# Optimization experiments

Measured on AMD Instinct MI355X. Metric: run time of the kernel, lower is better.

## Reference

```python
import jax, jax.numpy as jnp
import numpy as np

T, Z, Y, X = 16, 16, 16, 16
NS, NC = 4, 3
D = NS * NC  # 12 internal (spin*color) components
DIAG = 4.5   # 4 + mass
OUT_PARITY = 0


def _r_masks():
    t = jnp.arange(T).reshape(T, 1, 1, 1, 1)
    z = jnp.arange(Z).reshape(1, Z, 1, 1, 1)
    y = jnp.arange(Y).reshape(1, 1, Y, 1, 1)
    r = (t + z + y + OUT_PARITY) % 2
    r = jnp.broadcast_to(r, (T, Z, Y, X // 2, D))
    return r == 1, r == 0  # fwd mask, bwd mask


def _cmatvec(Kr, Ki, vr, vi):
    # complex (K) @ (v) per site; K: [T,Z,Y,X/2,D,D], v: [T,Z,Y,X/2,D]
    ar = jnp.einsum('tzyxij,tzyxj->tzyxi', Kr, vr) - jnp.einsum('tzyxij,tzyxj->tzyxi', Ki, vi)
    ai = jnp.einsum('tzyxij,tzyxj->tzyxi', Kr, vi) + jnp.einsum('tzyxij,tzyxj->tzyxi', Ki, vr)
    return ar, ai


def setup_inputs() -> dict:
    key = jax.random.key(0)
    ks = jax.random.split(key, 6)
    shp_psi = (T, Z, Y, X // 2, NS, NC)
    shp_K = (4, T, Z, Y, X // 2, D, D)
    return {
        'psi_re': jax.random.normal(ks[0], shp_psi, dtype=jnp.float32),
        'psi_im': jax.random.normal(ks[1], shp_psi, dtype=jnp.float32),
        'K_fwd_re': jax.random.normal(ks[2], shp_K, dtype=jnp.float32),
        'K_fwd_im': jax.random.normal(ks[3], shp_K, dtype=jnp.float32),
        'K_bwd_re': jax.random.normal(ks[4], shp_K, dtype=jnp.float32),
        'K_bwd_im': jax.random.normal(ks[5], shp_K, dtype=jnp.float32),
    }


def reference(psi_re, psi_im, K_fwd_re, K_fwd_im, K_bwd_re, K_bwd_im):
    pr = psi_re.reshape(T, Z, Y, X // 2, D)
    pi = psi_im.reshape(T, Z, Y, X // 2, D)
    mask_f, mask_b = _r_masks()
    out_re = DIAG * pr
    out_im = DIAG * pi
    for mu in range(4):
        ax = mu  # ldim = mu - 5 on a rank-5 tensor == axis mu
        if mu < 3:
            pf_re = jnp.roll(pr, -1, axis=ax); pf_im = jnp.roll(pi, -1, axis=ax)
            pb_re = jnp.roll(pr, 1, axis=ax); pb_im = jnp.roll(pi, 1, axis=ax)
        else:
            # staggered X hop on the half-lattice, selected by parity masks
            pf_re = jnp.where(mask_f, jnp.roll(pr, -1, axis=ax), pr)
            pf_im = jnp.where(mask_f, jnp.roll(pi, -1, axis=ax), pi)
            pb_re = jnp.where(mask_b, jnp.roll(pr, 1, axis=ax), pr)
            pb_im = jnp.where(mask_b, jnp.roll(pi, 1, axis=ax), pi)
        cf_re, cf_im = _cmatvec(K_fwd_re[mu], K_fwd_im[mu], pf_re, pf_im)
        cb_re, cb_im = _cmatvec(K_bwd_re[mu], K_bwd_im[mu], pb_re, pb_im)
        out_re = out_re - 0.5 * (cf_re + cb_re)
        out_im = out_im - 0.5 * (cf_im + cb_im)
    return (out_re.reshape(T, Z, Y, X // 2, NS, NC),
            out_im.reshape(T, Z, Y, X // 2, NS, NC))
```

## Files before the change

### kernel.cpp

```cpp
#include <hip/hip_runtime.h>

#define TD 16
#define ZD 16
#define YD 16
#define XH 8
#define DD 12
#define NSITES (TD*ZD*YD*XH)
#define SPB 16
#define THREADS (SPB*DD)
#define DIAG 4.5f
#define VSTRIDE 100

__global__ __launch_bounds__(THREADS) void hop_kernel(
    const float* __restrict__ psi_re, const float* __restrict__ psi_im,
    const float* __restrict__ K_fwd_re, const float* __restrict__ K_fwd_im,
    const float* __restrict__ K_bwd_re, const float* __restrict__ K_bwd_im,
    float* __restrict__ out_re, float* __restrict__ out_im)
{
    __shared__ float vre[SPB][VSTRIDE];
    __shared__ float vim[SPB][VSTRIDE];
    __shared__ int   nidx[SPB][8];

    const int tid   = threadIdx.x;
    const int site0 = blockIdx.x * SPB;

    if (tid < SPB * 8) {
        const int s = tid >> 3, c = tid & 7;
        const int sg = site0 + s;
        const int x = sg & 7, y = (sg >> 3) & 15, z = (sg >> 7) & 15, t = (sg >> 11) & 15;
        const int r = (t + z + y) & 1;
        int nt = t, nz = z, ny = y, nx = x;
        switch (c) {
            case 0: nt = (t + 1)  & 15; break;
            case 1: nt = (t + 15) & 15; break;
            case 2: nz = (z + 1)  & 15; break;
            case 3: nz = (z + 15) & 15; break;
            case 4: ny = (y + 1)  & 15; break;
            case 5: ny = (y + 15) & 15; break;
            case 6: if (r == 1) nx = (x + 1) & 7; break;
            case 7: if (r == 0) nx = (x + 7) & 7; break;
        }
        nidx[s][c] = ((nt * 16 + nz) * 16 + ny) * 8 + nx;
    }
    __syncthreads();

    for (int e = tid; e < SPB * 8 * DD; e += THREADS) {
        const int j  = e % 12;
        const int sc = e / 12;
        const int s  = sc >> 3, c = sc & 7;
        const int n  = nidx[s][c];
        vre[s][c * 12 + j] = psi_re[n * 12 + j];
        vim[s][c * 12 + j] = psi_im[n * 12 + j];
    }
    __syncthreads();

    const int s    = tid / 12;
    const int i    = tid - s * 12;
    const int site = site0 + s;

    const float pr_c = psi_re[site * 12 + i];
    const float pi_c = psi_im[site * 12 + i];
    float o_re = DIAG * pr_c;
    float o_im = DIAG * pi_c;

    #pragma unroll 2
    for (int c = 0; c < 8; ++c) {
        const int mu = c >> 1;
        const float* __restrict__ Kr_arr = (c & 1) ? K_bwd_re : K_fwd_re;
        const float* __restrict__ Ki_arr = (c & 1) ? K_bwd_im : K_fwd_im;
        const int off = (mu * NSITES + site) * 144 + i * 12;
        const float4* Kr4 = (const float4*)(Kr_arr + off);
        const float4* Ki4 = (const float4*)(Ki_arr + off);
        const float4 a0 = Kr4[0], a1 = Kr4[1], a2 = Kr4[2];
        const float4 b0 = Ki4[0], b1 = Ki4[1], b2 = Ki4[2];
        const float kr[12] = {a0.x,a0.y,a0.z,a0.w, a1.x,a1.y,a1.z,a1.w, a2.x,a2.y,a2.z,a2.w};
        const float ki[12] = {b0.x,b0.y,b0.z,b0.w, b1.x,b1.y,b1.z,b1.w, b2.x,b2.y,b2.z,b2.w};
        const float* __restrict__ vr = &vre[s][c * 12];
        const float* __restrict__ vi = &vim[s][c * 12];
        float sr = 0.f, si = 0.f;
        #pragma unroll
        for (int j = 0; j < 12; ++j) {
            const float krj = kr[j], kij = ki[j];
            const float vrj = vr[j], vij = vi[j];
            sr += krj * vrj - kij * vij;
            si += krj * vij + kij * vrj;
        }
        o_re -= 0.5f * sr;
        o_im -= 0.5f * si;
    }

    out_re[site * 12 + i] = o_re;
    out_im[site * 12 + i] = o_im;
}

extern "C" void kernel_launch(void* const* d_in, const int* in_sizes, int n_in,
                              void* d_out, int out_size, void* d_ws, size_t ws_size,
                              hipStream_t stream) {
    const float* psi_re   = (const float*)d_in[0];
    const float* psi_im   = (const float*)d_in[1];
    const float* K_fwd_re = (const float*)d_in[2];
    const float* K_fwd_im = (const float*)d_in[3];
    const float* K_bwd_re = (const float*)d_in[4];
    const float* K_bwd_im = (const float*)d_in[5];
    float* out_re = (float*)d_out;
    float* out_im = out_re + (out_size / 2);

    hop_kernel<<<NSITES / SPB, THREADS, 0, stream>>>(
        psi_re, psi_im, K_fwd_re, K_fwd_im, K_bwd_re, K_bwd_im, out_re, out_im);
}
```

Before: 274.0 us.

## Fuse neighbor index calc into gather and software-pipeline K loads

New measurement: 283.2 us. 1.03x slower.

```diff
diff --git a/kernel.cpp b/kernel.cpp
--- a/kernel.cpp
+++ b/kernel.cpp
@@ -10,8 +10,22 @@
 #define THREADS (SPB*DD)
 #define DIAG 4.5f
 #define VSTRIDE 100
+#define MU_STRIDE (NSITES*144)
 
-__global__ __launch_bounds__(THREADS) void hop_kernel(
+__device__ __forceinline__ void cdot4(const float4 kr, const float4 ki,
+                                      const float4 vr, const float4 vi,
+                                      float& sr, float& si) {
+    sr = fmaf(kr.x, vr.x, sr); sr = fmaf(-ki.x, vi.x, sr);
+    si = fmaf(kr.x, vi.x, si); si = fmaf(ki.x, vr.x, si);
+    sr = fmaf(kr.y, vr.y, sr); sr = fmaf(-ki.y, vi.y, sr);
+    si = fmaf(kr.y, vi.y, si); si = fmaf(ki.y, vr.y, si);
+    sr = fmaf(kr.z, vr.z, sr); sr = fmaf(-ki.z, vi.z, sr);
+    si = fmaf(kr.z, vi.z, si); si = fmaf(ki.z, vr.z, si);
+    sr = fmaf(kr.w, vr.w, sr); sr = fmaf(-ki.w, vi.w, sr);
+    si = fmaf(kr.w, vi.w, si); si = fmaf(ki.w, vr.w, si);
+}
+
+__global__ __launch_bounds__(THREADS, 4) void hop_kernel(
     const float* __restrict__ psi_re, const float* __restrict__ psi_im,
     const float* __restrict__ K_fwd_re, const float* __restrict__ K_fwd_im,
     const float* __restrict__ K_bwd_re, const float* __restrict__ K_bwd_im,
@@ -19,74 +33,79 @@
 {
     __shared__ float vre[SPB][VSTRIDE];
     __shared__ float vim[SPB][VSTRIDE];
-    __shared__ int   nidx[SPB][8];
 
     const int tid   = threadIdx.x;
     const int site0 = blockIdx.x * SPB;
 
-    if (tid < SPB * 8) {
-        const int s = tid >> 3, c = tid & 7;
+    const int jj  = tid % 12;
+    const int scb = tid / 12;
+    const int cc  = scb & 7;
+    const int sb  = scb >> 3;
+
+    const int dt = (cc == 0) - (cc == 1);
+    const int dz = (cc == 2) - (cc == 3);
+    const int dy = (cc == 4) - (cc == 5);
+
+    float tr[8], ti[8];
+    int   dst[8];
+    #pragma unroll
+    for (int k = 0; k < 8; ++k) {
+        const int s  = sb + 2 * k;
         const int sg = site0 + s;
         const int x = sg & 7, y = (sg >> 3) & 15, z = (sg >> 7) & 15, t = (sg >> 11) & 15;
         const int r = (t + z + y) & 1;
-        int nt = t, nz = z, ny = y, nx = x;
-        switch (c) {
-            case 0: nt = (t + 1)  & 15; break;
-            case 1: nt = (t + 15) & 15; break;
-            case 2: nz = (z + 1)  & 15; break;
-            case 3: nz = (z + 15) & 15; break;
-            case 4: ny = (y + 1)  & 15; break;
-            case 5: ny = (y + 15) & 15; break;
-            case 6: if (r == 1) nx = (x + 1) & 7; break;
-            case 7: if (r == 0) nx = (x + 7) & 7; break;
-        }
-        nidx[s][c] = ((nt * 16 + nz) * 16 + ny) * 8 + nx;
+        int dx = 0;
+        if (cc == 6) dx =  (r == 1);
+        if (cc == 7) dx = -(r == 0);
+        const int nt = (t + dt) & 15, nz = (z + dz) & 15,
+                  ny = (y + dy) & 15, nx = (x + dx) & 7;
+        const int n = ((nt * 16 + nz) * 16 + ny) * 8 + nx;
+        const int a = n * 12 + jj;
+        tr[k]  = psi_re[a];
+        ti[k]  = psi_im[a];
+        dst[k] = s * VSTRIDE + cc * 12 + jj;
+    }
+    #pragma unroll
+    for (int k = 0; k < 8; ++k) {
+        ((float*)vre)[dst[k]] = tr[k];
+        ((float*)vim)[dst[k]] = ti[k];
     }
     __syncthreads();
 
-    for (int e = tid; e < SPB * 8 * DD; e += THREADS) {
-        const int j  = e % 12;
-        const int sc = e / 12;
-        const int s  = sc >> 3, c = sc & 7;
-        const int n  = nidx[s][c];
-        vre[s][c * 12 + j] = psi_re[n * 12 + j];
-        vim[s][c * 12 + j] = psi_im[n * 12 + j];
-    }
-    __syncthreads();
-
-    const int s    = tid / 12;
-    const int i    = tid - s * 12;
-    const int site = site0 + s;
+    const int s      = scb;
+    const int i      = jj;
+    const int site   = site0 + s;
+    const int rowoff = site * 144 + i * 12;
 
     const float pr_c = psi_re[site * 12 + i];
     const float pi_c = psi_im[site * 12 + i];
     float o_re = DIAG * pr_c;
     float o_im = DIAG * pi_c;
 
-    #pragma unroll 2
+    #define KR(c) ((const float4*)((((c) & 1) ? K_bwd_re : K_fwd_re) + ((c) >> 1) * MU_STRIDE + rowoff))
+    #define KI(c) ((const float4*)((((c) & 1) ? K_bwd_im : K_fwd_im) + ((c) >> 1) * MU_STRIDE + rowoff))
+
+    float4 cr0 = KR(0)[0], cr1 = KR(0)[1], cr2 = KR(0)[2];
+    float4 ci0 = KI(0)[0], ci1 = KI(0)[1], ci2 = KI(0)[2];
+
+    #pragma unroll
     for (int c = 0; c < 8; ++c) {
-        const int mu = c >> 1;
-        const float* __restrict__ Kr_arr = (c & 1) ? K_bwd_re : K_fwd_re;
-        const float* __restrict__ Ki_arr = (c & 1) ? K_bwd_im : K_fwd_im;
-        const int off = (mu * NSITES + site) * 144 + i * 12;
-        const float4* Kr4 = (const float4*)(Kr_arr + off);
-        const float4* Ki4 = (const float4*)(Ki_arr + off);
-        const float4 a0 = Kr4[0], a1 = Kr4[1], a2 = Kr4[2];
-        const float4 b0 = Ki4[0], b1 = Ki4[1], b2 = Ki4[2];
-        const float kr[12] = {a0.x,a0.y,a0.z,a0.w, a1.x,a1.y,a1.z,a1.w, a2.x,a2.y,a2.z,a2.w};
-        const float ki[12] = {b0.x,b0.y,b0.z,b0.w, b1.x,b1.y,b1.z,b1.w, b2.x,b2.y,b2.z,b2.w};
-        const float* __restrict__ vr = &vre[s][c * 12];
-        const float* __restrict__ vi = &vim[s][c * 12];
+        float4 nr0, nr1, nr2, ni0, ni1, ni2;
+        if (c < 7) {
+            nr0 = KR(c + 1)[0]; nr1 = KR(c + 1)[1]; nr2 = KR(c + 1)[2];
+            ni0 = KI(c + 1)[0]; ni1 = KI(c + 1)[1]; ni2 = KI(c + 1)[2];
+        }
+        const float4* v4r = (const float4*)&vre[s][c * 12];
+        const float4* v4i = (const float4*)&vim[s][c * 12];
+        const float4 vr0 = v4r[0], vr1 = v4r[1], vr2 = v4r[2];
+        const float4 vi0 = v4i[0], vi1 = v4i[1], vi2 = v4i[2];
         float sr = 0.f, si = 0.f;
-        #pragma unroll
-        for (int j = 0; j < 12; ++j) {
-            const float krj = kr[j], kij = ki[j];
-            const float vrj = vr[j], vij = vi[j];
-            sr += krj * vrj - kij * vij;
-            si += krj * vij + kij * vrj;
-        }
+        cdot4(cr0, ci0, vr0, vi0, sr, si);
+        cdot4(cr1, ci1, vr1, vi1, sr, si);
+        cdot4(cr2, ci2, vr2, vi2, sr, si);
         o_re -= 0.5f * sr;
         o_im -= 0.5f * si;
+        if (c < 7) { cr0 = nr0; cr1 = nr1; cr2 = nr2; ci0 = ni0; ci1 = ni1; ci2 = ni2; }
     }
 
     out_re[site * 12 + i] = o_re;
```
